# Kernel tuning notes

Hardware: AMD Instinct MI355X
Metric: run time of the kernel (lower is better)

The kernel has to match this reference:

```python
import jax, jax.numpy as jnp
import numpy as np

PROJ_DIM = 512
HIDDEN_DIM = 1024
OUTPUT_DIM = 32000
BATCH = 256
TRG_LEN = 512


def setup_inputs() -> dict:
    key = jax.random.key(0)
    ks = jax.random.split(key, 10)
    H = PROJ_DIM
    inp = {
        "x": jax.random.normal(ks[0], (BATCH, TRG_LEN, 1), dtype=jnp.float32),
        "hidden": jnp.zeros((1, BATCH, H), dtype=jnp.float32),
        "trg": jax.random.randint(ks[1], (BATCH, TRG_LEN), 0, OUTPUT_DIM),
        # LSTM params (PyTorch layout, gate order i,f,g,o)
        "w_ih": jax.random.normal(ks[2], (4 * H, 1), dtype=jnp.float32) * (1.0 / np.sqrt(H)),
        "w_hh": jax.random.normal(ks[3], (4 * H, H), dtype=jnp.float32) * (1.0 / np.sqrt(H)),
        "b_ih": jax.random.normal(ks[4], (4 * H,), dtype=jnp.float32) * 0.01,
        "b_hh": jax.random.normal(ks[5], (4 * H,), dtype=jnp.float32) * 0.01,
        "fc1_w": jax.random.normal(ks[6], (HIDDEN_DIM, H), dtype=jnp.float32) * (1.0 / np.sqrt(H)),
        "fc1_b": jnp.zeros((HIDDEN_DIM,), dtype=jnp.float32),
        "fc2_w": jax.random.normal(ks[7], (OUTPUT_DIM, HIDDEN_DIM), dtype=jnp.float32) * (1.0 / np.sqrt(HIDDEN_DIM)),
        "fc2_b": jnp.zeros((OUTPUT_DIM,), dtype=jnp.float32),
    }
    return inp


def reference(x, hidden, trg, w_ih, w_hh, b_ih, b_hh, fc1_w, fc1_b, fc2_w, fc2_b):
    # hidden arg is ignored (source overwrites it with None). Teacher forcing
    # fixed to True: the fed-back argmax never affects LSTM state, and the
    # return value is only the output at the final timestep.
    B, T = trg.shape
    H = w_hh.shape[1]
    bias = b_ih + b_hh  # (4H,)
    # inputs fed at steps t=1..T-1 are trg[:, 0..T-2] as float scalars
    inputs = trg[:, : T - 1].astype(jnp.float32).T[..., None]  # (T-1, B, 1)

    def step(carry, x_t):
        h, c = carry  # (B, H) each
        gates = x_t @ w_ih.T + h @ w_hh.T + bias  # (B, 4H)
        i, f, g, o = jnp.split(gates, 4, axis=-1)
        i = jax.nn.sigmoid(i)
        f = jax.nn.sigmoid(f)
        g = jnp.tanh(g)
        o = jax.nn.sigmoid(o)
        c = f * c + i * g
        h = o * jnp.tanh(c)
        return (h, c), None

    h0 = jnp.zeros((B, H), dtype=jnp.float32)
    c0 = jnp.zeros((B, H), dtype=jnp.float32)
    (h_last, _), _ = jax.lax.scan(step, (h0, c0), inputs)

    # head applied to final timestep's LSTM output: fc2(relu(fc1(h)))
    z = jax.nn.relu(h_last @ fc1_w.T + fc1_b)  # (B, hidden_dim)
    out = z @ fc2_w.T + fc2_b  # (B, output_dim)
    return out
```

## Files before the change

### kernel.cpp

```cpp
#include <hip/hip_runtime.h>
#include <stdint.h>

typedef uint32_t u32;
typedef uint16_t u16;
typedef __attribute__((ext_vector_type(8))) short bf16x8;
typedef __attribute__((ext_vector_type(4))) float f32x4;

__device__ __forceinline__ u16 f2bf(float f) {
  u32 u = __builtin_bit_cast(u32, f);
  return (u16)((u + 0x7FFFu + ((u >> 16) & 1u)) >> 16);
}
__device__ __forceinline__ u32 pack2bf(float a, float b) {
  return (u32)f2bf(a) | ((u32)f2bf(b) << 16);
}
__device__ __forceinline__ uint4 pack8bf(float4 a, float4 b) {
  uint4 r;
  r.x = pack2bf(a.x, a.y); r.y = pack2bf(a.z, a.w);
  r.z = pack2bf(b.x, b.y); r.w = pack2bf(b.z, b.w);
  return r;
}
__device__ __forceinline__ float sigmoid_(float x) { return 1.0f / (1.0f + __expf(-x)); }
__device__ __forceinline__ float tanh_(float x) { return 1.0f - 2.0f / (1.0f + __expf(2.0f * x)); }

__global__ __launch_bounds__(256, 2) void lstm_kernel(
    const int* __restrict__ trg, const float* __restrict__ w_ih,
    const float* __restrict__ w_hh, const float* __restrict__ b_ih,
    const float* __restrict__ b_hh, u16* __restrict__ h_buf,
    int* __restrict__ flags) {
  __shared__ u16 Bb[16 * 520];
  __shared__ float Xl[16 * 513];
  __shared__ u32 Hs[256];
  const int tid = threadIdx.x;
  const int wave = tid >> 6, lane = tid & 63;
  const int q = lane >> 4, n = lane & 15;
  const int bg = blockIdx.x & 15, ug = blockIdx.x >> 4;

  #pragma unroll
  for (int c = 0; c < 4; ++c) {
    int e = c * 2048 + tid * 8;
    int rn = e >> 9, t0 = e & 511;
    const int* src = trg + (bg * 16 + rn) * 512 + t0;
    int4 a = *(const int4*)src;
    int4 b = *(const int4*)(src + 4);
    float* dst = &Xl[rn * 513 + t0];
    dst[0] = (float)a.x; dst[1] = (float)a.y; dst[2] = (float)a.z; dst[3] = (float)a.w;
    dst[4] = (float)b.x; dst[5] = (float)b.y; dst[6] = (float)b.z; dst[7] = (float)b.w;
  }

  bf16x8 Areg[2][16];
  const int rit = lane & 15;
  #pragma unroll
  for (int i = 0; i < 2; ++i) {
    int grow = (rit & 3) * 512 + ug * 32 + wave * 8 + 2 * (rit >> 2) + i;
    const float* wr = w_hh + (size_t)grow * 512;
    #pragma unroll
    for (int ks = 0; ks < 16; ++ks) {
      const float* p = wr + ks * 32 + q * 8;
      float4 f0 = *(const float4*)p;
      float4 f1 = *(const float4*)(p + 4);
      Areg[i][ks] = __builtin_bit_cast(bf16x8, pack8bf(f0, f1));
    }
  }

  float wi[2][4], bs[2][4];
  #pragma unroll
  for (int i = 0; i < 2; ++i) {
    #pragma unroll
    for (int r = 0; r < 4; ++r) {
      int grow = r * 512 + ug * 32 + wave * 8 + q * 2 + i;
      wi[i][r] = w_ih[grow];
      bs[i][r] = b_ih[grow] + b_hh[grow];
    }
  }
  float cst[2] = {0.f, 0.f};
  __syncthreads();

  for (int t = 1; t <= 511; ++t) {
    if (t > 1) {
      int cnt = 0;
      while (__hip_atomic_load(&flags[bg * 512 + (t - 1)], __ATOMIC_RELAXED,
                               __HIP_MEMORY_SCOPE_AGENT) < 16) {
        if (++cnt > (1 << 22)) break;
      }
    }
    {
      const u16* src = h_buf + (size_t)(((t - 1) & 1) * 16 + bg) * 8192;
      const u16* p0 = src + 0 * 2048 + tid * 8;
      const u16* p1 = src + 1 * 2048 + tid * 8;
      const u16* p2 = src + 2 * 2048 + tid * 8;
      const u16* p3 = src + 3 * 2048 + tid * 8;
      uint4 d0, d1, d2, d3;
      asm volatile(
          "global_load_dwordx4 %0, %4, off sc0 sc1\n\t"
          "global_load_dwordx4 %1, %5, off sc0 sc1\n\t"
          "global_load_dwordx4 %2, %6, off sc0 sc1\n\t"
          "global_load_dwordx4 %3, %7, off sc0 sc1\n\t"
          "s_waitcnt vmcnt(0)"
          : "=&v"(d0), "=&v"(d1), "=&v"(d2), "=&v"(d3)
          : "v"(p0), "v"(p1), "v"(p2), "v"(p3)
          : "memory");
      #pragma unroll
      for (int c = 0; c < 4; ++c) {
        int e = c * 2048 + tid * 8;
        int rn = e >> 9, k = e & 511;
        uint4 d = (c == 0) ? d0 : (c == 1) ? d1 : (c == 2) ? d2 : d3;
        *(uint4*)&Bb[rn * 520 + k] = d;
      }
    }
    __syncthreads();

    f32x4 acc[2] = {{0.f, 0.f, 0.f, 0.f}, {0.f, 0.f, 0.f, 0.f}};
    const u16* brow = &Bb[n * 520];
    #pragma unroll
    for (int ks = 0; ks < 16; ++ks) {
      bf16x8 bf = *(const bf16x8*)(brow + ks * 32 + q * 8);
      acc[0] = __builtin_amdgcn_mfma_f32_16x16x32_bf16(Areg[0][ks], bf, acc[0], 0, 0, 0);
      acc[1] = __builtin_amdgcn_mfma_f32_16x16x32_bf16(Areg[1][ks], bf, acc[1], 0, 0, 0);
    }

    float x = Xl[n * 513 + (t - 1)];
    float hv0, hv1;
    #pragma unroll
    for (int i = 0; i < 2; ++i) {
      float pi = acc[i][0] + x * wi[i][0] + bs[i][0];
      float pf = acc[i][1] + x * wi[i][1] + bs[i][1];
      float pg = acc[i][2] + x * wi[i][2] + bs[i][2];
      float po = acc[i][3] + x * wi[i][3] + bs[i][3];
      float ig = sigmoid_(pi), fg = sigmoid_(pf), og = sigmoid_(po);
      float gg = tanh_(pg);
      cst[i] = fg * cst[i] + ig * gg;
      float h = og * tanh_(cst[i]);
      if (i == 0) hv0 = h; else hv1 = h;
    }

    Hs[n * 16 + wave * 4 + q] = pack2bf(hv0, hv1);
    __syncthreads();
    {
      u32 hv = Hs[tid];
      u32* dst = (u32*)h_buf + (size_t)((t & 1) ? 65536 : 0) +
                 (size_t)(bg * 16 + (tid >> 4)) * 256 + ug * 16 + (tid & 15);
      asm volatile("global_store_dword %0, %1, off sc1\n\ts_waitcnt vmcnt(0)"
                   :: "v"(dst), "v"(hv) : "memory");
    }
    __syncthreads();
    if (tid == 0) {
      __hip_atomic_fetch_add(&flags[bg * 512 + t], 1, __ATOMIC_RELAXED,
                             __HIP_MEMORY_SCOPE_AGENT);
    }
  }
}

__global__ __launch_bounds__(256, 1) void head_gemm(
    const float* __restrict__ A, const u16* __restrict__ B,
    const float* __restrict__ bias, void* __restrict__ outv,
    int M, int K, int mode) {
  __shared__ u16 Ach[128 * 40];
  __shared__ u16 Bch[256 * 40];
  const int tid = threadIdx.x;
  const int wave = tid >> 6, lane = tid & 63;
  const int q = lane >> 4, l15 = lane & 15;
  const int mblk = blockIdx.x * 128;
  const int nch = K >> 5;
  f32x4 acc[2][16];
  #pragma unroll
  for (int i = 0; i < 2; ++i)
    #pragma unroll
    for (int nb = 0; nb < 16; ++nb) acc[i][nb] = (f32x4){0.f, 0.f, 0.f, 0.f};

  for (int ch = 0; ch < nch; ++ch) {
    __syncthreads();
    {
      int row = tid >> 1, k = (tid & 1) * 16;
      const float* src = A + (size_t)(mblk + row) * K + ch * 32 + k;
      float4 f0 = *(const float4*)src;
      float4 f1 = *(const float4*)(src + 4);
      float4 f2 = *(const float4*)(src + 8);
      float4 f3 = *(const float4*)(src + 12);
      u16* dst = &Ach[row * 40 + k];
      *(uint4*)dst = pack8bf(f0, f1);
      *(uint4*)(dst + 8) = pack8bf(f2, f3);
    }
    #pragma unroll
    for (int c = 0; c < 4; ++c) {
      int e = c * 2048 + tid * 8;
      int nr = e >> 5, k = e & 31;
      uint4 d = *(const uint4*)(B + (size_t)nr * K + ch * 32 + k);
      *(uint4*)&Bch[nr * 40 + k] = d;
    }
    __syncthreads();
    bf16x8 a0 = *(const bf16x8*)&Ach[((wave * 2 + 0) * 16 + l15) * 40 + q * 8];
    bf16x8 a1 = *(const bf16x8*)&Ach[((wave * 2 + 1) * 16 + l15) * 40 + q * 8];
    #pragma unroll
    for (int nb = 0; nb < 16; ++nb) {
      bf16x8 bf = *(const bf16x8*)&Bch[(nb * 16 + l15) * 40 + q * 8];
      acc[0][nb] = __builtin_amdgcn_mfma_f32_16x16x32_bf16(a0, bf, acc[0][nb], 0, 0, 0);
      acc[1][nb] = __builtin_amdgcn_mfma_f32_16x16x32_bf16(a1, bf, acc[1][nb], 0, 0, 0);
    }
  }
  #pragma unroll
  for (int i = 0; i < 2; ++i) {
    int j0 = mblk + (wave * 2 + i) * 16 + q * 4;
    float4 bv = *(const float4*)(bias + j0);
    #pragma unroll
    for (int nb = 0; nb < 16; ++nb) {
      int b = nb * 16 + l15;
      f32x4 v = acc[i][nb];
      v[0] += bv.x; v[1] += bv.y; v[2] += bv.z; v[3] += bv.w;
      if (mode == 0) {
        v[0] = fmaxf(v[0], 0.f); v[1] = fmaxf(v[1], 0.f);
        v[2] = fmaxf(v[2], 0.f); v[3] = fmaxf(v[3], 0.f);
        u16* z = (u16*)outv;
        uint2 pk;
        pk.x = pack2bf(v[0], v[1]);
        pk.y = pack2bf(v[2], v[3]);
        *(uint2*)(z + (size_t)b * M + j0) = pk;
      } else {
        float* op = (float*)outv + (size_t)b * M + j0;
        float4 o;
        o.x = v[0]; o.y = v[1]; o.z = v[2]; o.w = v[3];
        *(float4*)op = o;
      }
    }
  }
}

extern "C" void kernel_launch(void* const* d_in, const int* in_sizes, int n_in,
                              void* d_out, int out_size, void* d_ws, size_t ws_size,
                              hipStream_t stream) {
  (void)in_sizes; (void)n_in; (void)out_size; (void)ws_size;
  const int* trg = (const int*)d_in[2];
  const float* w_ih = (const float*)d_in[3];
  const float* w_hh = (const float*)d_in[4];
  const float* b_ih = (const float*)d_in[5];
  const float* b_hh = (const float*)d_in[6];
  const float* fc1_w = (const float*)d_in[7];
  const float* fc1_b = (const float*)d_in[8];
  const float* fc2_w = (const float*)d_in[9];
  const float* fc2_b = (const float*)d_in[10];

  u16* h_buf = (u16*)d_ws;
  int* flags = (int*)((char*)d_ws + 524288);
  u16* z = (u16*)((char*)d_ws + 557056);

  hipMemsetAsync(d_ws, 0, 262144, stream);
  hipMemsetAsync((char*)d_ws + 524288, 0, 32768, stream);

  lstm_kernel<<<256, 256, 0, stream>>>(trg, w_ih, w_hh, b_ih, b_hh, h_buf, flags);

  const u16* h_final = h_buf + 131072;
  head_gemm<<<8, 256, 0, stream>>>(fc1_w, h_final, fc1_b, (void*)z, 1024, 512, 0);
  head_gemm<<<250, 256, 0, stream>>>(fc2_w, z, fc2_b, d_out, 32000, 1024, 1);
}
```

Before: 1.503 ms.

## Halve LSTM block count by giving each block twice the hidden units

Each persistent LSTM block now owns 64 hidden units instead of 32, holding four register-resident bf16 W_hh fragments per lane, so the grid shrinks from 256 to 128 blocks and each batch group waits on 8 producer flags per step instead of 16. The aim is to cut the per-timestep cross-block synchronisation and flag-polling cost, which dominates this sequential recurrence. In exchange each block does twice the MFMA and gate work per step, and register pressure roughly doubles (launch bounds drop to one block per SM), which lengthens the per-step critical path.

```diff
diff --git a/kernel.cpp b/kernel.cpp
--- a/kernel.cpp
+++ b/kernel.cpp
@@ -22,14 +22,14 @@
 __device__ __forceinline__ float sigmoid_(float x) { return 1.0f / (1.0f + __expf(-x)); }
 __device__ __forceinline__ float tanh_(float x) { return 1.0f - 2.0f / (1.0f + __expf(2.0f * x)); }
 
-__global__ __launch_bounds__(256, 2) void lstm_kernel(
+__global__ __launch_bounds__(256, 1) void lstm_kernel(
     const int* __restrict__ trg, const float* __restrict__ w_ih,
     const float* __restrict__ w_hh, const float* __restrict__ b_ih,
     const float* __restrict__ b_hh, u16* __restrict__ h_buf,
     int* __restrict__ flags) {
   __shared__ u16 Bb[16 * 520];
   __shared__ float Xl[16 * 513];
-  __shared__ u32 Hs[256];
+  __shared__ u32 Hs[16 * 34];
   const int tid = threadIdx.x;
   const int wave = tid >> 6, lane = tid & 63;
   const int q = lane >> 4, n = lane & 15;
@@ -47,11 +47,12 @@
     dst[4] = (float)b.x; dst[5] = (float)b.y; dst[6] = (float)b.z; dst[7] = (float)b.w;
   }
 
-  bf16x8 Areg[2][16];
+  bf16x8 Areg[4][16];
   const int rit = lane & 15;
   #pragma unroll
-  for (int i = 0; i < 2; ++i) {
-    int grow = (rit & 3) * 512 + ug * 32 + wave * 8 + 2 * (rit >> 2) + i;
+  for (int i = 0; i < 4; ++i) {
+    int grow = (rit & 3) * 512 + ug * 64 + wave * 16 + 8 * (i >> 1) +
+               2 * (rit >> 2) + (i & 1);
     const float* wr = w_hh + (size_t)grow * 512;
     #pragma unroll
     for (int ks = 0; ks < 16; ++ks) {
@@ -62,24 +63,24 @@
     }
   }
 
-  float wi[2][4], bs[2][4];
-  #pragma unroll
-  for (int i = 0; i < 2; ++i) {
+  float wi[4][4], bs[4][4];
+  #pragma unroll
+  for (int i = 0; i < 4; ++i) {
     #pragma unroll
     for (int r = 0; r < 4; ++r) {
-      int grow = r * 512 + ug * 32 + wave * 8 + q * 2 + i;
+      int grow = r * 512 + ug * 64 + wave * 16 + 8 * (i >> 1) + 2 * q + (i & 1);
       wi[i][r] = w_ih[grow];
       bs[i][r] = b_ih[grow] + b_hh[grow];
     }
   }
-  float cst[2] = {0.f, 0.f};
+  float cst[4] = {0.f, 0.f, 0.f, 0.f};
   __syncthreads();
 
   for (int t = 1; t <= 511; ++t) {
     if (t > 1) {
       int cnt = 0;
       while (__hip_atomic_load(&flags[bg * 512 + (t - 1)], __ATOMIC_RELAXED,
-                               __HIP_MEMORY_SCOPE_AGENT) < 16) {
+                               __HIP_MEMORY_SCOPE_AGENT) < 8) {
         if (++cnt > (1 << 22)) break;
       }
     }
@@ -109,19 +110,22 @@
     }
     __syncthreads();
 
-    f32x4 acc[2] = {{0.f, 0.f, 0.f, 0.f}, {0.f, 0.f, 0.f, 0.f}};
+    f32x4 acc[4] = {{0.f, 0.f, 0.f, 0.f}, {0.f, 0.f, 0.f, 0.f},
+                    {0.f, 0.f, 0.f, 0.f}, {0.f, 0.f, 0.f, 0.f}};
     const u16* brow = &Bb[n * 520];
     #pragma unroll
     for (int ks = 0; ks < 16; ++ks) {
       bf16x8 bf = *(const bf16x8*)(brow + ks * 32 + q * 8);
       acc[0] = __builtin_amdgcn_mfma_f32_16x16x32_bf16(Areg[0][ks], bf, acc[0], 0, 0, 0);
       acc[1] = __builtin_amdgcn_mfma_f32_16x16x32_bf16(Areg[1][ks], bf, acc[1], 0, 0, 0);
+      acc[2] = __builtin_amdgcn_mfma_f32_16x16x32_bf16(Areg[2][ks], bf, acc[2], 0, 0, 0);
+      acc[3] = __builtin_amdgcn_mfma_f32_16x16x32_bf16(Areg[3][ks], bf, acc[3], 0, 0, 0);
     }
 
     float x = Xl[n * 513 + (t - 1)];
-    float hv0, hv1;
-    #pragma unroll
-    for (int i = 0; i < 2; ++i) {
+    float hv[4];
+    #pragma unroll
+    for (int i = 0; i < 4; ++i) {
       float pi = acc[i][0] + x * wi[i][0] + bs[i][0];
       float pf = acc[i][1] + x * wi[i][1] + bs[i][1];
       float pg = acc[i][2] + x * wi[i][2] + bs[i][2];
@@ -129,18 +133,19 @@
       float ig = sigmoid_(pi), fg = sigmoid_(pf), og = sigmoid_(po);
       float gg = tanh_(pg);
       cst[i] = fg * cst[i] + ig * gg;
-      float h = og * tanh_(cst[i]);
-      if (i == 0) hv0 = h; else hv1 = h;
-    }
-
-    Hs[n * 16 + wave * 4 + q] = pack2bf(hv0, hv1);
+      hv[i] = og * tanh_(cst[i]);
+    }
+
+    Hs[n * 34 + wave * 8 + q] = pack2bf(hv[0], hv[1]);
+    Hs[n * 34 + wave * 8 + 4 + q] = pack2bf(hv[2], hv[3]);
     __syncthreads();
     {
-      u32 hv = Hs[tid];
+      int nr = tid >> 4, k2 = (tid & 15) * 2;
+      uint2 hv2 = *(const uint2*)&Hs[nr * 34 + k2];
       u32* dst = (u32*)h_buf + (size_t)((t & 1) ? 65536 : 0) +
-                 (size_t)(bg * 16 + (tid >> 4)) * 256 + ug * 16 + (tid & 15);
-      asm volatile("global_store_dword %0, %1, off sc1\n\ts_waitcnt vmcnt(0)"
-                   :: "v"(dst), "v"(hv) : "memory");
+                 (size_t)(bg * 16 + nr) * 256 + ug * 32 + k2;
+      asm volatile("global_store_dwordx2 %0, %1, off sc1\n\ts_waitcnt vmcnt(0)"
+                   :: "v"(dst), "v"(hv2) : "memory");
     }
     __syncthreads();
     if (tid == 0) {
@@ -245,7 +250,7 @@
   hipMemsetAsync(d_ws, 0, 262144, stream);
   hipMemsetAsync((char*)d_ws + 524288, 0, 32768, stream);
 
-  lstm_kernel<<<256, 256, 0, stream>>>(trg, w_ih, w_hh, b_ih, b_hh, h_buf, flags);
+  lstm_kernel<<<128, 256, 0, stream>>>(trg, w_ih, w_hh, b_ih, b_hh, h_buf, flags);
 
   const u16* h_final = h_buf + 131072;
   head_gemm<<<8, 256, 0, stream>>>(fc1_w, h_final, fc1_b, (void*)z, 1024, 512, 0);
```

Result: slower. 1.941 ms (+29.1%).

## Split LSTM batch groups to 8 rows across 512 blocks with monotonic counters

Applied to the files above, without the earlier changes.

Doubles the persistent LSTM grid from 256 to 512 blocks, with each block handling 8 batch rows instead of 16, so each step's per-block work and h loads shrink. Per-timestep flag slots are replaced by one monotonically increasing counter per batch group, padded to separate cache lines, and waiters spin until it reaches 16*(t-1). A block-index XOR swizzle changes how groups map to blocks. The MFMA still runs on 16 columns with rows duplicated, so half its compute is wasted. The design also depends on all 512 blocks being co-resident (launch bounds allow 2 per CU) and adds more spinning blocks per group.

```diff
diff --git a/kernel.cpp b/kernel.cpp
--- a/kernel.cpp
+++ b/kernel.cpp
@@ -27,19 +27,21 @@
     const float* __restrict__ w_hh, const float* __restrict__ b_ih,
     const float* __restrict__ b_hh, u16* __restrict__ h_buf,
     int* __restrict__ flags) {
-  __shared__ u16 Bb[16 * 520];
-  __shared__ float Xl[16 * 513];
-  __shared__ u32 Hs[256];
+  __shared__ u16 Bb[8 * 520];
+  __shared__ float Xl[8 * 513];
+  __shared__ u32 Hs[128];
   const int tid = threadIdx.x;
   const int wave = tid >> 6, lane = tid & 63;
   const int q = lane >> 4, n = lane & 15;
-  const int bg = blockIdx.x & 15, ug = blockIdx.x >> 4;
-
-  #pragma unroll
-  for (int c = 0; c < 4; ++c) {
+  const int m = n & 7;
+  const int j = blockIdx.x ^ ((blockIdx.x >> 8) & 1);
+  const int bgr = j & 31, ug = j >> 5;
+
+  #pragma unroll
+  for (int c = 0; c < 2; ++c) {
     int e = c * 2048 + tid * 8;
     int rn = e >> 9, t0 = e & 511;
-    const int* src = trg + (bg * 16 + rn) * 512 + t0;
+    const int* src = trg + (bgr * 8 + rn) * 512 + t0;
     int4 a = *(const int4*)src;
     int4 b = *(const int4*)(src + 4);
     float* dst = &Xl[rn * 513 + t0];
@@ -77,40 +79,38 @@
 
   for (int t = 1; t <= 511; ++t) {
     if (t > 1) {
+      const int need = (t - 1) << 4;
       int cnt = 0;
-      while (__hip_atomic_load(&flags[bg * 512 + (t - 1)], __ATOMIC_RELAXED,
-                               __HIP_MEMORY_SCOPE_AGENT) < 16) {
+      while (__hip_atomic_load(&flags[bgr * 128], __ATOMIC_RELAXED,
+                               __HIP_MEMORY_SCOPE_AGENT) < need) {
         if (++cnt > (1 << 22)) break;
       }
     }
     {
-      const u16* src = h_buf + (size_t)(((t - 1) & 1) * 16 + bg) * 8192;
-      const u16* p0 = src + 0 * 2048 + tid * 8;
-      const u16* p1 = src + 1 * 2048 + tid * 8;
-      const u16* p2 = src + 2 * 2048 + tid * 8;
-      const u16* p3 = src + 3 * 2048 + tid * 8;
-      uint4 d0, d1, d2, d3;
+      const u16* src = h_buf + (size_t)(((t - 1) & 1) * 16 + (bgr >> 1)) * 8192 +
+                       (bgr & 1) * 4096;
+      const u16* p0 = src + tid * 8;
+      const u16* p1 = src + 2048 + tid * 8;
+      uint4 d0, d1;
       asm volatile(
-          "global_load_dwordx4 %0, %4, off sc0 sc1\n\t"
-          "global_load_dwordx4 %1, %5, off sc0 sc1\n\t"
-          "global_load_dwordx4 %2, %6, off sc0 sc1\n\t"
-          "global_load_dwordx4 %3, %7, off sc0 sc1\n\t"
+          "global_load_dwordx4 %0, %2, off sc0 sc1\n\t"
+          "global_load_dwordx4 %1, %3, off sc0 sc1\n\t"
           "s_waitcnt vmcnt(0)"
-          : "=&v"(d0), "=&v"(d1), "=&v"(d2), "=&v"(d3)
-          : "v"(p0), "v"(p1), "v"(p2), "v"(p3)
+          : "=&v"(d0), "=&v"(d1)
+          : "v"(p0), "v"(p1)
           : "memory");
       #pragma unroll
-      for (int c = 0; c < 4; ++c) {
+      for (int c = 0; c < 2; ++c) {
         int e = c * 2048 + tid * 8;
         int rn = e >> 9, k = e & 511;
-        uint4 d = (c == 0) ? d0 : (c == 1) ? d1 : (c == 2) ? d2 : d3;
+        uint4 d = (c == 0) ? d0 : d1;
         *(uint4*)&Bb[rn * 520 + k] = d;
       }
     }
     __syncthreads();
 
     f32x4 acc[2] = {{0.f, 0.f, 0.f, 0.f}, {0.f, 0.f, 0.f, 0.f}};
-    const u16* brow = &Bb[n * 520];
+    const u16* brow = &Bb[m * 520];
     #pragma unroll
     for (int ks = 0; ks < 16; ++ks) {
       bf16x8 bf = *(const bf16x8*)(brow + ks * 32 + q * 8);
@@ -118,7 +118,7 @@
       acc[1] = __builtin_amdgcn_mfma_f32_16x16x32_bf16(Areg[1][ks], bf, acc[1], 0, 0, 0);
     }
 
-    float x = Xl[n * 513 + (t - 1)];
+    float x = Xl[m * 513 + (t - 1)];
     float hv0, hv1;
     #pragma unroll
     for (int i = 0; i < 2; ++i) {
@@ -133,18 +133,19 @@
       if (i == 0) hv0 = h; else hv1 = h;
     }
 
-    Hs[n * 16 + wave * 4 + q] = pack2bf(hv0, hv1);
-    __syncthreads();
-    {
+    if (n < 8) Hs[m * 16 + wave * 4 + q] = pack2bf(hv0, hv1);
+    __syncthreads();
+    if (tid < 128) {
       u32 hv = Hs[tid];
       u32* dst = (u32*)h_buf + (size_t)((t & 1) ? 65536 : 0) +
-                 (size_t)(bg * 16 + (tid >> 4)) * 256 + ug * 16 + (tid & 15);
+                 (size_t)((bgr >> 1) * 16 + (bgr & 1) * 8 + (tid >> 4)) * 256 +
+                 ug * 16 + (tid & 15);
       asm volatile("global_store_dword %0, %1, off sc1\n\ts_waitcnt vmcnt(0)"
                    :: "v"(dst), "v"(hv) : "memory");
     }
     __syncthreads();
     if (tid == 0) {
-      __hip_atomic_fetch_add(&flags[bg * 512 + t], 1, __ATOMIC_RELAXED,
+      __hip_atomic_fetch_add(&flags[bgr * 128], 1, __ATOMIC_RELAXED,
                              __HIP_MEMORY_SCOPE_AGENT);
     }
   }
@@ -245,7 +246,7 @@
   hipMemsetAsync(d_ws, 0, 262144, stream);
   hipMemsetAsync((char*)d_ws + 524288, 0, 32768, stream);
 
-  lstm_kernel<<<256, 256, 0, stream>>>(trg, w_ih, w_hh, b_ih, b_hh, h_buf, flags);
+  lstm_kernel<<<512, 256, 0, stream>>>(trg, w_ih, w_hh, b_ih, b_hh, h_buf, flags);
 
   const u16* h_final = h_buf + 131072;
   head_gemm<<<8, 256, 0, stream>>>(fc1_w, h_final, fc1_b, (void*)z, 1024, 512, 0);
```

New measurement: 2.031 ms. 1.35x slower.
